# Optimization experiments

Hardware: AMD Instinct MI355X
Metric: run time of the kernel (lower is better)

The kernel has to match this reference:

```python
import jax, jax.numpy as jnp
import numpy as np

NUM_EMBEDDINGS = 1024
EMBEDDING_DIM = 64
BETA = 0.25  # commitment_cost


def setup_inputs() -> dict:
    key = jax.random.key(0)
    k1, k2 = jax.random.split(key)
    z = jax.random.normal(k1, (32, EMBEDDING_DIM, 32, 32), dtype=jnp.float32)
    embedding = jax.random.normal(k2, (NUM_EMBEDDINGS, EMBEDDING_DIM), dtype=jnp.float32)
    return {"z": z, "embedding": embedding}


def reference(z, embedding):
    B, D, H, W = z.shape
    beta = jnp.asarray(BETA, z.dtype)
    # [B, D, H, W] -> [B*H*W, D]
    z_flat = jnp.transpose(z, (0, 2, 3, 1)).reshape(-1, D)
    # squared L2 distances to each code: ||z||^2 - 2 z.e^T + ||e||^2  -> [N, E]
    dist = (
        jnp.sum(z_flat * z_flat, axis=1, keepdims=True)
        - 2.0 * (z_flat @ embedding.T)
        + jnp.sum(embedding * embedding, axis=1)
    )
    encoding_indices = jnp.argmin(dist, axis=1)  # [N]
    # direct gather instead of one-hot matmul (same math)
    quantized = embedding[encoding_indices]  # [N, D]
    quantized = jnp.transpose(quantized.reshape(B, H, W, D), (0, 3, 1, 2))
    commitment_loss = beta * jnp.mean(
        (jax.lax.stop_gradient(z) - quantized) ** 2
    )
    codebook_loss = jnp.mean((z - jax.lax.stop_gradient(quantized)) ** 2)
    loss = commitment_loss + codebook_loss
    # straight-through estimator
    quantized_st = z + jax.lax.stop_gradient(quantized - z)
    return (quantized_st, loss, encoding_indices)
```

## Files before the change

### kernel.cpp

```cpp
#include <hip/hip_runtime.h>

typedef __attribute__((ext_vector_type(8))) short short8;
typedef __attribute__((ext_vector_type(4))) float f32x4;
typedef unsigned int uint32;

#define QOUT 2097152

__device__ __forceinline__ unsigned short f2bf(float f){
  uint32 u = __float_as_uint(f);
  return (unsigned short)((u + 0x7FFFu + ((u >> 16) & 1u)) >> 16);
}
__device__ __forceinline__ float bf2f(unsigned short h){
  return __uint_as_float(((uint32)h) << 16);
}
__device__ __forceinline__ uint32 med3u(uint32 a, uint32 b, uint32 c){
  uint32 d;
  asm("v_med3_u32 %0, %1, %2, %3" : "=v"(d) : "v"(a), "v"(b), "v"(c));
  return d;
}

__global__ void vq_prep(const float* __restrict__ emb, unsigned char* __restrict__ ebg,
                        float* __restrict__ nrm64, int* __restrict__ cnt){
  int u = blockIdx.x * 256 + threadIdx.x;
  if (u == 0) *cnt = 0;
  int C = u >> 3, oct = u & 7;
  const float4* e4 = reinterpret_cast<const float4*>(emb) + C * 16 + oct * 2;
  float4 v0 = e4[0], v1 = e4[1];
  float vv[8] = {v0.x, v0.y, v0.z, v0.w, v1.x, v1.y, v1.z, v1.w};
  float s = 0.f;
  short8 H, L;
#pragma unroll
  for (int j = 0; j < 8; ++j){
    float v = vv[j];
    s = fmaf(v, v, s);
    unsigned short hs = f2bf(v);
    unsigned short ls = f2bf(v - bf2f(hs));
    H[j] = (short)hs; L[j] = (short)ls;
  }
  int ng = C >> 4, c15 = C & 15, kf = oct >> 2, gg = oct & 3;
  unsigned char* base = ebg + ng * 4096 + kf * 2048 + (gg * 16 + c15) * 16;
  *reinterpret_cast<short8*>(base) = H;
  *reinterpret_cast<short8*>(base + 1024) = L;
#pragma unroll
  for (int d = 1; d < 8; d <<= 1) s += __shfl_xor(s, d);
  if (oct == 0) nrm64[C] = 0.5f * s + 128.0f;
}

__global__ __launch_bounds__(256, 2) void vq_main(
    const float* __restrict__ z, const float* __restrict__ emb,
    const unsigned char* __restrict__ ebg, const float* __restrict__ nrm64,
    float* __restrict__ out, float* __restrict__ partial, int* __restrict__ cnt)
{
  __shared__ float zf[64 * 68];
  __shared__ float nrmlds[1024];
  __shared__ uint32 mg[64][2][3];
  __shared__ uint32 cand[64][4];
  __shared__ int kidx[64];
  __shared__ float werr[4];
  __shared__ float red[256];
  __shared__ int isLast;

  const int t = threadIdx.x;
  const int bi = blockIdx.x;
  const int n0 = bi * 64;
  const int b = n0 >> 10;
  const int hw0 = n0 & 1023;
  const int w = t >> 6, lane = t & 63;
  const int wm = w >> 1, wn = w & 1;
  const int l15 = lane & 15, g = lane >> 4;

#pragma unroll
  for (int i = 0; i < 4; ++i) nrmlds[i * 256 + t] = nrm64[i * 256 + t];

#pragma unroll
  for (int k = 0; k < 16; ++k){
    int li = k * 256 + t;
    int d = li >> 6, j = li & 63;
    zf[j * 68 + d] = z[((b * 64 + d) << 10) + hw0 + j];
  }
  __syncthreads();

  short8 ah[2][2], al[2][2];
#pragma unroll
  for (int mf = 0; mf < 2; ++mf)
#pragma unroll
    for (int kf = 0; kf < 2; ++kf){
      int row = wm * 32 + mf * 16 + l15;
      int base = row * 68 + kf * 32 + g * 8;
      float4 q0 = *reinterpret_cast<float4*>(&zf[base]);
      float4 q1 = *reinterpret_cast<float4*>(&zf[base + 4]);
      float vv[8] = {q0.x,q0.y,q0.z,q0.w,q1.x,q1.y,q1.z,q1.w};
#pragma unroll
      for (int j = 0; j < 8; ++j){
        float v = -vv[j];
        unsigned short hs = f2bf(v);
        unsigned short ls = f2bf(v - bf2f(hs));
        ah[mf][kf][j] = (short)hs;
        al[mf][kf][j] = (short)ls;
      }
    }

  uint32 u0[8], u1[8], u2[8];
#pragma unroll
  for (int s = 0; s < 8; ++s){ u0[s] = 0xFFFFFFFFu; u1[s] = 0xFFFFFFFFu; u2[s] = 0xFFFFFFFFu; }

  const unsigned char* pbase = ebg + (wn << 17) + (lane << 4);
  short8 fb[4][4];

#pragma unroll
  for (int s = 0; s < 3; ++s){
    const unsigned char* p = pbase + (s << 12);
    fb[s][0] = *reinterpret_cast<const short8*>(p);
    fb[s][1] = *reinterpret_cast<const short8*>(p + 1024);
    fb[s][2] = *reinterpret_cast<const short8*>(p + 2048);
    fb[s][3] = *reinterpret_cast<const short8*>(p + 3072);
  }

#pragma unroll
  for (int i = 0; i < 32; ++i){
    if (i < 29){
      const unsigned char* p = pbase + ((i + 3) << 12);
      fb[(i + 3) & 3][0] = *reinterpret_cast<const short8*>(p);
      fb[(i + 3) & 3][1] = *reinterpret_cast<const short8*>(p + 1024);
      fb[(i + 3) & 3][2] = *reinterpret_cast<const short8*>(p + 2048);
      fb[(i + 3) & 3][3] = *reinterpret_cast<const short8*>(p + 3072);
    }
    short8 bh0 = fb[i & 3][0];
    short8 bl0 = fb[i & 3][1];
    short8 bh1 = fb[i & 3][2];
    short8 bl1 = fb[i & 3][3];
    int code = ((wn * 32 + i) << 4) + l15;
    float nv = nrmlds[code];
    f32x4 a0 = {nv, nv, nv, nv};
    f32x4 a1 = {nv, nv, nv, nv};
    a0 = __builtin_amdgcn_mfma_f32_16x16x32_bf16(ah[0][0], bh0, a0, 0,0,0);
    a0 = __builtin_amdgcn_mfma_f32_16x16x32_bf16(ah[0][1], bh1, a0, 0,0,0);
    a0 = __builtin_amdgcn_mfma_f32_16x16x32_bf16(al[0][0], bh0, a0, 0,0,0);
    a0 = __builtin_amdgcn_mfma_f32_16x16x32_bf16(al[0][1], bh1, a0, 0,0,0);
    a0 = __builtin_amdgcn_mfma_f32_16x16x32_bf16(ah[0][0], bl0, a0, 0,0,0);
    a0 = __builtin_amdgcn_mfma_f32_16x16x32_bf16(ah[0][1], bl1, a0, 0,0,0);
    a1 = __builtin_amdgcn_mfma_f32_16x16x32_bf16(ah[1][0], bh0, a1, 0,0,0);
    a1 = __builtin_amdgcn_mfma_f32_16x16x32_bf16(ah[1][1], bh1, a1, 0,0,0);
    a1 = __builtin_amdgcn_mfma_f32_16x16x32_bf16(al[1][0], bh0, a1, 0,0,0);
    a1 = __builtin_amdgcn_mfma_f32_16x16x32_bf16(al[1][1], bh1, a1, 0,0,0);
    a1 = __builtin_amdgcn_mfma_f32_16x16x32_bf16(ah[1][0], bl0, a1, 0,0,0);
    a1 = __builtin_amdgcn_mfma_f32_16x16x32_bf16(ah[1][1], bl1, a1, 0,0,0);
    uint32 kb = (uint32)code;
#pragma unroll
    for (int r = 0; r < 4; ++r){
      uint32 k0v = (__float_as_uint(a0[r]) & 0xFFFFFC00u) | kb;
      u2[r] = med3u(k0v, u1[r], u2[r]);
      u1[r] = med3u(k0v, u0[r], u1[r]);
      u0[r] = u0[r] < k0v ? u0[r] : k0v;
      uint32 k1v = (__float_as_uint(a1[r]) & 0xFFFFFC00u) | kb;
      u2[4+r] = med3u(k1v, u1[4+r], u2[4+r]);
      u1[4+r] = med3u(k1v, u0[4+r], u1[4+r]);
      u0[4+r] = u0[4+r] < k1v ? u0[4+r] : k1v;
    }
  }

#pragma unroll
  for (int dm = 1; dm < 16; dm <<= 1){
#pragma unroll
    for (int s = 0; s < 8; ++s){
      uint32 x0 = (uint32)__shfl_xor((int)u0[s], dm);
      uint32 x1 = (uint32)__shfl_xor((int)u1[s], dm);
      uint32 x2 = (uint32)__shfl_xor((int)u2[s], dm);
      u2[s] = med3u(x0, u1[s], u2[s]); u1[s] = med3u(x0, u0[s], u1[s]); u0[s] = u0[s] < x0 ? u0[s] : x0;
      u2[s] = med3u(x1, u1[s], u2[s]); u1[s] = med3u(x1, u0[s], u1[s]); u0[s] = u0[s] < x1 ? u0[s] : x1;
      u2[s] = med3u(x2, u1[s], u2[s]); u1[s] = med3u(x2, u0[s], u1[s]); u0[s] = u0[s] < x2 ? u0[s] : x2;
    }
  }
  if (l15 == 0){
#pragma unroll
    for (int mf = 0; mf < 2; ++mf)
#pragma unroll
      for (int r = 0; r < 4; ++r){
        int lr = wm * 32 + mf * 16 + g * 4 + r;
        int s = mf * 4 + r;
        mg[lr][wn][0] = u0[s]; mg[lr][wn][1] = u1[s]; mg[lr][wn][2] = u2[s];
      }
  }
  __syncthreads();

  if (t < 64){
    uint32 a0k = mg[t][0][0], a1k = mg[t][0][1], a2k = mg[t][0][2];
#pragma unroll
    for (int j2 = 0; j2 < 3; ++j2){
      uint32 x = mg[t][1][j2];
      a2k = med3u(x, a1k, a2k); a1k = med3u(x, a0k, a1k); a0k = a0k < x ? a0k : x;
    }
    kidx[t] = (int)(a0k & 1023u);
    float d0 = __uint_as_float(a0k & 0xFFFFFC00u);
    float d1 = __uint_as_float(a1k & 0xFFFFFC00u);
    cand[t][0] = a0k; cand[t][1] = a1k; cand[t][2] = a2k;
    cand[t][3] = (d1 - d0 < 0.0625f) ? 1u : 0u;
  }
  __syncthreads();

  {
    int row = t >> 2, j = t & 3;
    if (cand[row][3]){
      double s = 1e300; int myk = 0x7FFFFFFF;
      if (j < 3){
        int k = (int)(cand[row][j] & 1023u);
        const float* e = emb + k * 64;
        double acc = 0.0;
        for (int d = 0; d < 64; ++d){
          double df = (double)zf[row * 68 + d] - (double)e[d];
          acc += df * df;
        }
        s = acc; myk = k;
      }
#pragma unroll
      for (int dx = 1; dx < 4; dx <<= 1){
        double so = __shfl_xor(s, dx);
        int ko = __shfl_xor(myk, dx);
        if (so < s || (so == s && ko < myk)) { s = so; myk = ko; }
      }
      if (j == 0) kidx[row] = myk;
    }
  }
  __syncthreads();

  {
    int row = t & 63, dp = t >> 6;
    int k = kidx[row];
    const float* e = emb + k * 64;
    float* ob = out + (b << 16) + hw0 + row;
    float err = 0.f;
#pragma unroll
    for (int dd = 0; dd < 16; ++dd){
      int d = dp * 16 + dd;
      float zv = zf[row * 68 + d];
      float qv = e[d];
      ob[d << 10] = qv;
      float df = zv - qv;
      err = fmaf(df, df, err);
    }
    if (dp == 0) out[QOUT + 1 + n0 + row] = (float)k;
#pragma unroll
    for (int dx = 1; dx < 64; dx <<= 1) err += __shfl_xor(err, dx);
    if (lane == 0) werr[w] = err;
  }
  __syncthreads();
  if (t == 0){
    partial[bi] = (werr[0] + werr[1]) + (werr[2] + werr[3]);
    __threadfence();
    int pos = atomicAdd(cnt, 1);
    isLast = (pos == 511) ? 1 : 0;
  }
  __syncthreads();

  if (isLast){
    __threadfence();
    const volatile float* vp = partial;
    red[t] = vp[t] + vp[t + 256];
    __syncthreads();
    for (int ww = 128; ww > 0; ww >>= 1){
      if (t < ww) red[t] += red[t + ww];
      __syncthreads();
    }
    if (t == 0) out[QOUT] = 1.25f * red[0] * (1.0f / 2097152.0f);
  }
}

extern "C" void kernel_launch(void* const* d_in, const int* in_sizes, int n_in,
                              void* d_out, int out_size, void* d_ws, size_t ws_size,
                              hipStream_t stream) {
  const float* z   = (const float*)d_in[0];
  const float* emb = (const float*)d_in[1];
  float* out = (float*)d_out;
  unsigned char* ebg = (unsigned char*)d_ws;
  float* nrm64   = (float*)(ebg + 262144);
  float* partial = nrm64 + 1024;
  int*   cnt     = (int*)(partial + 512);

  vq_prep <<<32,  256, 0, stream>>>(emb, ebg, nrm64, cnt);
  vq_main <<<512, 256, 0, stream>>>(z, emb, ebg, nrm64, out, partial, cnt);
}
```

Before: 44.43 us.

## Compact flagged rows for wave-parallel fp64 rescoring, shrink prefetch depth, vectorize gather

Rows whose top-two bf16-split distances are close are now pushed into a compact shared-memory list with an atomic counter. Each wave then rescores one flagged row in fp64, with 16 lanes per candidate reading float4 slices of the codebook and reducing through shuffles. Previously four threads per row each looped serially over all 64 dimensions. The codebook fragment prefetch drops from three stages ahead to two, with a sched_barrier added, which cuts register pressure at the risk of exposing more load latency. The final gather now reads embedding rows as float4 vectors instead of scalar loads.

```diff
diff --git a/kernel.cpp b/kernel.cpp
--- a/kernel.cpp
+++ b/kernel.cpp
@@ -54,8 +54,10 @@
   __shared__ float zf[64 * 68];
   __shared__ float nrmlds[1024];
   __shared__ uint32 mg[64][2][3];
-  __shared__ uint32 cand[64][4];
+  __shared__ uint32 cand[64][3];
   __shared__ int kidx[64];
+  __shared__ int flagrow[64];
+  __shared__ int nflag;
   __shared__ float werr[4];
   __shared__ float red[256];
   __shared__ int isLast;
@@ -71,6 +73,7 @@
 
 #pragma unroll
   for (int i = 0; i < 4; ++i) nrmlds[i * 256 + t] = nrm64[i * 256 + t];
+  if (t == 255) nflag = 0;
 
 #pragma unroll
   for (int k = 0; k < 16; ++k){
@@ -105,10 +108,10 @@
   for (int s = 0; s < 8; ++s){ u0[s] = 0xFFFFFFFFu; u1[s] = 0xFFFFFFFFu; u2[s] = 0xFFFFFFFFu; }
 
   const unsigned char* pbase = ebg + (wn << 17) + (lane << 4);
-  short8 fb[4][4];
-
-#pragma unroll
-  for (int s = 0; s < 3; ++s){
+  short8 fb[3][4];
+
+#pragma unroll
+  for (int s = 0; s < 2; ++s){
     const unsigned char* p = pbase + (s << 12);
     fb[s][0] = *reinterpret_cast<const short8*>(p);
     fb[s][1] = *reinterpret_cast<const short8*>(p + 1024);
@@ -118,17 +121,18 @@
 
 #pragma unroll
   for (int i = 0; i < 32; ++i){
-    if (i < 29){
-      const unsigned char* p = pbase + ((i + 3) << 12);
-      fb[(i + 3) & 3][0] = *reinterpret_cast<const short8*>(p);
-      fb[(i + 3) & 3][1] = *reinterpret_cast<const short8*>(p + 1024);
-      fb[(i + 3) & 3][2] = *reinterpret_cast<const short8*>(p + 2048);
-      fb[(i + 3) & 3][3] = *reinterpret_cast<const short8*>(p + 3072);
-    }
-    short8 bh0 = fb[i & 3][0];
-    short8 bl0 = fb[i & 3][1];
-    short8 bh1 = fb[i & 3][2];
-    short8 bl1 = fb[i & 3][3];
+    if (i < 30){
+      const unsigned char* p = pbase + ((i + 2) << 12);
+      fb[(i + 2) % 3][0] = *reinterpret_cast<const short8*>(p);
+      fb[(i + 2) % 3][1] = *reinterpret_cast<const short8*>(p + 1024);
+      fb[(i + 2) % 3][2] = *reinterpret_cast<const short8*>(p + 2048);
+      fb[(i + 2) % 3][3] = *reinterpret_cast<const short8*>(p + 3072);
+    }
+    __builtin_amdgcn_sched_barrier(0);
+    short8 bh0 = fb[i % 3][0];
+    short8 bl0 = fb[i % 3][1];
+    short8 bh1 = fb[i % 3][2];
+    short8 bl1 = fb[i % 3][3];
     int code = ((wn * 32 + i) << 4) + l15;
     float nv = nrmlds[code];
     f32x4 a0 = {nv, nv, nv, nv};
@@ -191,34 +195,46 @@
       a2k = med3u(x, a1k, a2k); a1k = med3u(x, a0k, a1k); a0k = a0k < x ? a0k : x;
     }
     kidx[t] = (int)(a0k & 1023u);
+    cand[t][0] = a0k; cand[t][1] = a1k; cand[t][2] = a2k;
     float d0 = __uint_as_float(a0k & 0xFFFFFC00u);
     float d1 = __uint_as_float(a1k & 0xFFFFFC00u);
-    cand[t][0] = a0k; cand[t][1] = a1k; cand[t][2] = a2k;
-    cand[t][3] = (d1 - d0 < 0.0625f) ? 1u : 0u;
+    if (d1 - d0 < 0.0625f){
+      int pos = atomicAdd(&nflag, 1);
+      flagrow[pos] = t;
+    }
   }
   __syncthreads();
 
   {
-    int row = t >> 2, j = t & 3;
-    if (cand[row][3]){
-      double s = 1e300; int myk = 0x7FFFFFFF;
-      if (j < 3){
-        int k = (int)(cand[row][j] & 1023u);
-        const float* e = emb + k * 64;
-        double acc = 0.0;
-        for (int d = 0; d < 64; ++d){
-          double df = (double)zf[row * 68 + d] - (double)e[d];
-          acc += df * df;
-        }
-        s = acc; myk = k;
+    int nf = nflag;
+    int cidx = lane >> 4, q = lane & 15;
+    for (int n = w; n < nf; n += 4){
+      int row = flagrow[n];
+      double acc = 0.0;
+      if (cidx < 3){
+        int k = (int)(cand[row][cidx] & 1023u);
+        float4 ev = *reinterpret_cast<const float4*>(emb + k * 64 + q * 4);
+        float4 zv = *reinterpret_cast<const float4*>(&zf[row * 68 + q * 4]);
+        double d0v = (double)zv.x - (double)ev.x;
+        double d1v = (double)zv.y - (double)ev.y;
+        double d2v = (double)zv.z - (double)ev.z;
+        double d3v = (double)zv.w - (double)ev.w;
+        acc = d0v*d0v + d1v*d1v + d2v*d2v + d3v*d3v;
       }
 #pragma unroll
-      for (int dx = 1; dx < 4; dx <<= 1){
-        double so = __shfl_xor(s, dx);
-        int ko = __shfl_xor(myk, dx);
-        if (so < s || (so == s && ko < myk)) { s = so; myk = ko; }
+      for (int dx = 1; dx < 16; dx <<= 1) acc += __shfl_xor(acc, dx);
+      double s0 = __shfl(acc, 0);
+      double s1 = __shfl(acc, 16);
+      double s2 = __shfl(acc, 32);
+      if (lane == 0){
+        int k0 = (int)(cand[row][0] & 1023u);
+        int k1 = (int)(cand[row][1] & 1023u);
+        int k2 = (int)(cand[row][2] & 1023u);
+        int bk = k0; double bs = s0;
+        if (s1 < bs || (s1 == bs && k1 < bk)) { bs = s1; bk = k1; }
+        if (s2 < bs || (s2 == bs && k2 < bk)) { bs = s2; bk = k2; }
+        kidx[row] = bk;
       }
-      if (j == 0) kidx[row] = myk;
     }
   }
   __syncthreads();
@@ -226,14 +242,17 @@
   {
     int row = t & 63, dp = t >> 6;
     int k = kidx[row];
-    const float* e = emb + k * 64;
+    const float4* e4p = reinterpret_cast<const float4*>(emb + k * 64 + dp * 16);
+    float4 ev0 = e4p[0], ev1 = e4p[1], ev2 = e4p[2], ev3 = e4p[3];
+    float evf[16] = {ev0.x,ev0.y,ev0.z,ev0.w, ev1.x,ev1.y,ev1.z,ev1.w,
+                     ev2.x,ev2.y,ev2.z,ev2.w, ev3.x,ev3.y,ev3.z,ev3.w};
     float* ob = out + (b << 16) + hw0 + row;
     float err = 0.f;
 #pragma unroll
     for (int dd = 0; dd < 16; ++dd){
       int d = dp * 16 + dd;
       float zv = zf[row * 68 + d];
-      float qv = e[d];
+      float qv = evf[dd];
       ob[d << 10] = qv;
       float df = zv - qv;
       err = fmaf(df, df, err);
```

Result: faster. 43.46 us (-2.2%).
